# Kernel optimization log

Hardware: AMD Instinct MI355X
Metric: run time of the kernel (lower is better)

Reference implementation:

```python
import jax, jax.numpy as jnp
import numpy as np

N_FFT = 2048
HOP = 441
WIN_SIZE = 7
PAD = WIN_SIZE // 2
NP_WIN = WIN_SIZE * WIN_SIZE
COV_NORM = NP_WIN / (NP_WIN - 1.0)  # sample covariance, skimage default
DATA_RANGE = 2.0  # skimage float dtype_range (-1,1)
C1 = (0.01 * DATA_RANGE) ** 2
C2 = (0.03 * DATA_RANGE) ** 2
EPS = 1e-8

# periodic hann window (librosa fftbins=True)
_HANN = 0.5 - 0.5 * np.cos(2.0 * np.pi * np.arange(N_FFT) / N_FFT)


def wav_to_spectrogram(x):
    # x: [B, C, S] -> magnitude spectrogram [B, C, T, F]
    pad = N_FFT // 2
    xp = jnp.pad(x, ((0, 0), (0, 0), (pad, pad)), mode='reflect')  # torch 'reflect'
    L = xp.shape[-1]
    n_frames = (L - N_FFT) // HOP + 1
    idx = jnp.arange(n_frames)[:, None] * HOP + jnp.arange(N_FFT)[None, :]
    frames = xp[..., idx] * jnp.asarray(_HANN, xp.dtype)  # [B,C,T,N_FFT]
    spec = jnp.fft.rfft(frames, axis=-1)
    mag = jnp.sqrt(jnp.maximum(spec.real ** 2 + spec.imag ** 2, EPS))
    return mag


def _umean_last(x):
    # 1D uniform mean filter (size 7) along last axis, scipy 'reflect' boundary
    xp = jnp.pad(x, [(0, 0)] * (x.ndim - 1) + [(PAD, PAD)], mode='symmetric')
    cs = jnp.cumsum(xp, axis=-1)
    zero = jnp.zeros(cs.shape[:-1] + (1,), cs.dtype)
    cs = jnp.concatenate([zero, cs], axis=-1)
    return (cs[..., WIN_SIZE:] - cs[..., :-WIN_SIZE]) / WIN_SIZE


def umean2d(x):
    # separable 7x7 uniform filter over last two axes
    x = _umean_last(x)
    x = jnp.swapaxes(_umean_last(jnp.swapaxes(x, -1, -2)), -1, -2)
    return x


def ssim_map_mean(X, Y):
    ux, uy = umean2d(X), umean2d(Y)
    uxx, uyy, uxy = umean2d(X * X), umean2d(Y * Y), umean2d(X * Y)
    vx = COV_NORM * (uxx - ux * ux)
    vy = COV_NORM * (uyy - uy * uy)
    vxy = COV_NORM * (uxy - ux * uy)
    S = ((2 * ux * uy + C1) * (2 * vxy + C2)) / ((ux * ux + uy * uy + C1) * (vx + vy + C2))
    # crop pad on each side (skimage) then mean over the spatial map
    return jnp.mean(S[..., PAD:-PAD, PAD:-PAD], axis=(-2, -1))


def setup_inputs() -> dict:
    key = jax.random.key(0)
    k1, k2 = jax.random.split(key)
    B, C, S = 32, 2, 176400
    output = jax.random.normal(k1, (B, C, S), dtype=jnp.float32)
    target = jax.random.normal(k2, (B, C, S), dtype=jnp.float32)
    return {"output": output, "target": target}


def reference(output, target):
    so = wav_to_spectrogram(output)
    st = wav_to_spectrogram(target)
    res = ssim_map_mean(so, st)  # [B, C]
    return res[..., None, None]  # [B, C, 1, 1]
```

## Files before the change

kernel.cpp:

```cpp
#include <hip/hip_runtime.h>
#include <math.h>

#ifndef M_PI
#define M_PI 3.14159265358979323846
#endif

constexpr int S_LEN    = 176400;
constexpr int NFFT     = 2048;
constexpr int NC       = 1024;
constexpr int HOP_     = 441;
constexpr int T_FRAMES = 401;
constexpr int F_BINS   = 1025;
constexpr int F_STRIDE = 1028;
constexpr int N_CH     = 64;
constexpr float EPS_   = 1e-8f;
constexpr float C1_    = 0.0004f;
constexpr float C2_    = 0.0036f;
constexpr float COV_NORM_ = 49.0f / 48.0f;

constexpr int WIN_OFF  = 0;
constexpr int TWG_OFF  = 2048;
constexpr int UTW_OFF  = 3584;
constexpr int SPEC_OFF = 5696;

constexpr int ROWS_PW   = 16;
constexpr int NCHUNKS_R = 25;
constexpr int BANDS     = 5;
constexpr int BAND_ADV  = 248;

__device__ __forceinline__ int phys(int i) { return i ^ ((i >> 2) & 15) ^ ((i >> 6) & 15); }

__device__ __forceinline__ float2 cadd(float2 a, float2 b){ return make_float2(a.x+b.x, a.y+b.y); }
__device__ __forceinline__ float2 csub(float2 a, float2 b){ return make_float2(a.x-b.x, a.y-b.y); }
__device__ __forceinline__ float2 cmul(float2 a, float2 b){ return make_float2(a.x*b.x-a.y*b.y, a.x*b.y+a.y*b.x); }

__global__ __launch_bounds__(256) void init_tables_kernel(float* __restrict__ ws, float* __restrict__ out) {
    const int idx = blockIdx.x * 256 + threadIdx.x;
    if (idx < 64) out[idx] = 0.0f;
    if (idx < NFFT) {
        ws[WIN_OFF + idx] = 0.5f - 0.5f * cosf((float)(2.0 * M_PI / NFFT) * (float)idx);
    }
    if (idx < 768) {
        float ang = -2.0f * (float)M_PI * (float)idx / (float)NC;
        float s, c; sincosf(ang, &s, &c);
        ws[TWG_OFF + 2*idx] = c; ws[TWG_OFF + 2*idx+1] = s;
    }
    if (idx < F_BINS) {
        float ang = -(float)M_PI * (float)idx / (float)NC;
        float s, c; sincosf(ang, &s, &c);
        ws[UTW_OFF + 2*idx] = c; ws[UTW_OFF + 2*idx+1] = s;
    }
}

__device__ __forceinline__ void r4_dif_inplace(
    float2* __restrict__ A, int r0, int r1, int r2, int r3,
    float2 w1, float2 w2, float2 w3, bool tw)
{
    float2 x0c = A[r0];
    float2 x1c = A[r1];
    float2 x2c = A[r2];
    float2 x3c = A[r3];

    float2 a = cadd(x0c, x2c);
    float2 b = csub(x0c, x2c);
    float2 c = cadd(x1c, x3c);
    float2 d = csub(x1c, x3c);

    float2 y0 = cadd(a, c);
    float2 y2 = csub(a, c);
    float2 y1 = make_float2(b.x + d.y, b.y - d.x);
    float2 y3 = make_float2(b.x - d.y, b.y + d.x);

    A[r0] = y0;
    A[r1] = tw ? cmul(y1, w1) : y1;
    A[r2] = tw ? cmul(y2, w2) : y2;
    A[r3] = tw ? cmul(y3, w3) : y3;
}

__global__ __launch_bounds__(256, 8) void stft_mag_kernel(
    const float* __restrict__ x0, const float* __restrict__ x1,
    float* __restrict__ ws, int ch0, int nch, int swizzle)
{
    __shared__ float2 buf[2 * NC];

    const int tid = threadIdx.x;

    int ch, t;
    if (swizzle) {
        int g = blockIdx.x;
        ch = ch0 + (g & 7) * 8 + ((g >> 3) & 7);
        t  = g >> 6;
    } else {
        t  = blockIdx.x;
        ch = ch0 + blockIdx.y;
    }

    const float* __restrict__ xin0 = x0 + (size_t)ch * S_LEN;
    const float* __restrict__ xin1 = x1 + (size_t)ch * S_LEN;
    const float*  __restrict__ win = ws + WIN_OFF;
    const float2* __restrict__ twg = (const float2*)(ws + TWG_OFF);
    const float2* __restrict__ utw = (const float2*)(ws + UTW_OFF);

    const int base = t * HOP_ - NFFT / 2;
    float* fA0 = (float*)buf;
    float* fA1 = (float*)(buf + NC);
    if (base >= 0 && base + NFFT <= S_LEN) {
        #pragma unroll
        for (int k = 0; k < NFFT / 256; ++k) {
            int n = k * 256 + tid;
            int j = base + n;
            float w = win[n];
            int p = 2 * phys(n >> 1) + (n & 1);
            fA0[p] = xin0[j] * w;
            fA1[p] = xin1[j] * w;
        }
    } else {
        #pragma unroll
        for (int k = 0; k < NFFT / 256; ++k) {
            int n = k * 256 + tid;
            int j = base + n;
            j = (j < 0) ? -j : j;
            j = (j >= S_LEN) ? (2 * S_LEN - 2 - j) : j;
            float w = win[n];
            int p = 2 * phys(n >> 1) + (n & 1);
            fA0[p] = xin0[j] * w;
            fA1[p] = xin1[j] * w;
        }
    }
    __syncthreads();

    #pragma unroll
    for (int s = 0; s < 5; ++s) {
        const int M  = 256 >> (2 * s);
        const int q  = tid & (M - 1);
        const int e  = q << (2 * s);
        const int i0 = 4 * (tid - q) + q;

        const int r0 = phys(i0);
        const int r1 = phys(i0 + M);
        const int r2 = phys(i0 + 2 * M);
        const int r3 = phys(i0 + 3 * M);

        float2 w1, w2, w3;
        if (s < 4) {
            w1 = twg[e];
            w2 = twg[2 * e];
            w3 = twg[3 * e];
        } else {
            w1 = w2 = w3 = make_float2(1.0f, 0.0f);
        }

        r4_dif_inplace(buf,      r0, r1, r2, r3, w1, w2, w3, s < 4);
        r4_dif_inplace(buf + NC, r0, r1, r2, r3, w1, w2, w3, s < 4);

        __syncthreads();
    }

    const size_t perT = (size_t)T_FRAMES * F_STRIDE;
    float* __restrict__ sout0 =
        ws + SPEC_OFF + (size_t)(ch - ch0) * perT + (size_t)t * F_STRIDE;
    float* __restrict__ sout1 = sout0 + (size_t)nch * perT;

    const int R8 = ((tid & 3) << 6) | ((tid & 12) << 2) | ((tid >> 2) & 12) | ((tid >> 6) & 3);

    #pragma unroll
    for (int k = 0; k < 5; ++k) {
        int r = k * 256 + tid;
        if (k < 4 || tid == 0) {
            const int ra = (k < 4) ? ((R8 << 2) | k) : 0;
            const int rn = (NC - r) & (NC - 1);
            const int rb = ((rn & 3) << 8) | ((rn & 12) << 4) | (rn & 48)
                         | ((rn >> 4) & 12) | ((rn >> 8) & 3);
            const int ia = phys(ra);
            const int ib = phys(rb);
            float2 wu = utw[r];

            {
                float2 Zr = buf[ia];
                float2 Zn = buf[ib];
                float Ex = 0.5f * (Zr.x + Zn.x);
                float Ey = 0.5f * (Zr.y - Zn.y);
                float Ox = 0.5f * (Zr.y + Zn.y);
                float Oy = 0.5f * (Zn.x - Zr.x);
                float Xx = Ex + wu.x * Ox - wu.y * Oy;
                float Xy = Ey + wu.x * Oy + wu.y * Ox;
                sout0[r] = sqrtf(fmaxf(Xx * Xx + Xy * Xy, EPS_));
            }
            {
                float2 Zr = buf[NC + ia];
                float2 Zn = buf[NC + ib];
                float Ex = 0.5f * (Zr.x + Zn.x);
                float Ey = 0.5f * (Zr.y - Zn.y);
                float Ox = 0.5f * (Zr.y + Zn.y);
                float Oy = 0.5f * (Zn.x - Zr.x);
                float Xx = Ex + wu.x * Ox - wu.y * Oy;
                float Xy = Ey + wu.x * Oy + wu.y * Ox;
                sout1[r] = sqrtf(fmaxf(Xx * Xx + Xy * Xy, EPS_));
            }
        }
    }
}

#define HWIN7(sarr, W) {                                                     \
    float p0 = sarr[0], p01 = p0 + sarr[1], p012 = p01 + sarr[2],            \
          P = p012 + sarr[3];                                                \
    float a1 = __shfl_down(p012, 1, 64);                                     \
    float A1 = __shfl_down(P,    1, 64);                                     \
    float b0 = __shfl_down(p0,   2, 64);                                     \
    float b1 = __shfl_down(p01,  2, 64);                                     \
    W[0] = P + a1;                                                           \
    W[1] = P - p0 + A1;                                                      \
    W[2] = W[1] - sarr[1] + b0;                                              \
    W[3] = W[2] - sarr[2] + (b1 - b0);                                       \
}

__global__ __launch_bounds__(256) void ssim_kernel(
    const float* __restrict__ ws, float* __restrict__ out,
    int ch0, int nch)
{
    const int tid  = threadIdx.x;
    const int wid  = blockIdx.x * 4 + (tid >> 6);
    const int lane = tid & 63;
    const int total = nch * BANDS * NCHUNKS_R;
    if (wid >= total) return;

    const int cg    = wid / (BANDS * NCHUNKS_R);
    const int rem   = wid - cg * (BANDS * NCHUNKS_R);
    const int band  = rem / NCHUNKS_R;
    const int chunk = rem - band * NCHUNKS_R;

    const int t0 = 3 + chunk * ROWS_PW;
    const int t1 = min(t0 + ROWS_PW, T_FRAMES - 3);

    const int cb = band * BAND_ADV;
    int c4 = cb + 4 * lane;
    if (c4 > 1024) c4 = 1024;

    const size_t perT = (size_t)T_FRAMES * F_STRIDE;
    const float* __restrict__ X = ws + SPEC_OFF + (size_t)cg * perT + c4;
    const float* __restrict__ Y = ws + SPEC_OFF + ((size_t)nch + cg) * perT + c4;

    const int  fo      = cb + 3 + 4 * lane;
    const bool lane_ok = (lane <= 61);
    const float inv49  = 1.0f / 49.0f;

    float sx[4] = {0,0,0,0}, sy[4] = {0,0,0,0}, sxx[4] = {0,0,0,0},
          syy[4] = {0,0,0,0}, sxy[4] = {0,0,0,0};

    for (int rr = t0 - 3; rr < t0 + 3; ++rr) {
        float4 xv = *(const float4*)(X + (size_t)rr * F_STRIDE);
        float4 yv = *(const float4*)(Y + (size_t)rr * F_STRIDE);
        float xa[4] = {xv.x, xv.y, xv.z, xv.w}, ya[4] = {yv.x, yv.y, yv.z, yv.w};
        #pragma unroll
        for (int c = 0; c < 4; ++c) {
            sx[c] += xa[c]; sy[c] += ya[c];
            sxx[c] += xa[c]*xa[c]; syy[c] += ya[c]*ya[c]; sxy[c] += xa[c]*ya[c];
        }
    }

    double acc = 0.0;

    #pragma unroll 1
    for (int t = t0; t < t1; ++t) {
        {
            float4 xv = *(const float4*)(X + (size_t)(t + 3) * F_STRIDE);
            float4 yv = *(const float4*)(Y + (size_t)(t + 3) * F_STRIDE);
            float xa[4] = {xv.x, xv.y, xv.z, xv.w}, ya[4] = {yv.x, yv.y, yv.z, yv.w};
            #pragma unroll
            for (int c = 0; c < 4; ++c) {
                sx[c] += xa[c]; sy[c] += ya[c];
                sxx[c] += xa[c]*xa[c]; syy[c] += ya[c]*ya[c]; sxy[c] += xa[c]*ya[c];
            }
        }

        float wx[4], wy[4], wxx[4], wyy[4], wxy[4];
        HWIN7(sx,  wx);
        HWIN7(sy,  wy);
        HWIN7(sxx, wxx);
        HWIN7(syy, wyy);
        HWIN7(sxy, wxy);

        #pragma unroll
        for (int c = 0; c < 4; ++c) {
            if (lane_ok && (fo + c <= 1021)) {
                float ux  = wx[c]  * inv49, uy  = wy[c]  * inv49;
                float uxx = wxx[c] * inv49, uyy = wyy[c] * inv49, uxy = wxy[c] * inv49;
                float vx  = COV_NORM_ * (uxx - ux * ux);
                float vy  = COV_NORM_ * (uyy - uy * uy);
                float vxy = COV_NORM_ * (uxy - ux * uy);
                float Sv = ((2.f * ux * uy + C1_) * (2.f * vxy + C2_)) /
                           ((ux * ux + uy * uy + C1_) * (vx + vy + C2_));
                acc += (double)Sv;
            }
        }

        {
            float4 xv = *(const float4*)(X + (size_t)(t - 3) * F_STRIDE);
            float4 yv = *(const float4*)(Y + (size_t)(t - 3) * F_STRIDE);
            float xa[4] = {xv.x, xv.y, xv.z, xv.w}, ya[4] = {yv.x, yv.y, yv.z, yv.w};
            #pragma unroll
            for (int c = 0; c < 4; ++c) {
                sx[c] -= xa[c]; sy[c] -= ya[c];
                sxx[c] -= xa[c]*xa[c]; syy[c] -= ya[c]*ya[c]; sxy[c] -= xa[c]*ya[c];
            }
        }
    }

    #pragma unroll
    for (int off = 32; off > 0; off >>= 1) acc += __shfl_down(acc, off, 64);
    if (lane == 0) {
        atomicAdd(&out[ch0 + cg], (float)(acc / (395.0 * 1019.0)));
    }
}

extern "C" void kernel_launch(void* const* d_in, const int* in_sizes, int n_in,
                              void* d_out, int out_size, void* d_ws, size_t ws_size,
                              hipStream_t stream) {
    const float* x0 = (const float*)d_in[0];
    const float* x1 = (const float*)d_in[1];
    float* out = (float*)d_out;
    float* ws  = (float*)d_ws;

    const size_t table_bytes  = (size_t)SPEC_OFF * sizeof(float);
    const size_t per_ch_bytes = (size_t)2 * T_FRAMES * F_STRIDE * sizeof(float);
    int G = (int)((ws_size - table_bytes) / per_ch_bytes);
    if (G > N_CH) G = N_CH;
    if (G < 1)    G = 1;

    init_tables_kernel<<<dim3(16), dim3(256), 0, stream>>>(ws, out);

    for (int ch0 = 0; ch0 < N_CH; ch0 += G) {
        const int nch = (N_CH - ch0 < G) ? (N_CH - ch0) : G;

        if (nch == 64) {
            stft_mag_kernel<<<dim3(T_FRAMES * 64), dim3(256), 0, stream>>>(x0, x1, ws, ch0, nch, 1);
        } else {
            stft_mag_kernel<<<dim3(T_FRAMES, nch), dim3(256), 0, stream>>>(x0, x1, ws, ch0, nch, 0);
        }

        const int nwaves = nch * BANDS * NCHUNKS_R;
        ssim_kernel<<<dim3((nwaves + 3) / 4), dim3(256), 0, stream>>>(ws, out, ch0, nch);
    }
}
```

Before: 370.8 us.

## Keep sliding-window rows in a register ring and prefetch next row in SSIM kernel

```diff
diff --git a/kernel.cpp b/kernel.cpp
--- a/kernel.cpp
+++ b/kernel.cpp
@@ -23,8 +23,8 @@
 constexpr int UTW_OFF  = 3584;
 constexpr int SPEC_OFF = 5696;
 
-constexpr int ROWS_PW   = 16;
-constexpr int NCHUNKS_R = 25;
+constexpr int ROWS_PW   = 24;
+constexpr int NCHUNKS_R = 17;
 constexpr int BANDS     = 5;
 constexpr int BAND_ADV  = 248;
 
@@ -246,8 +246,11 @@
 
     float sx[4] = {0,0,0,0}, sy[4] = {0,0,0,0}, sxx[4] = {0,0,0,0},
           syy[4] = {0,0,0,0}, sxy[4] = {0,0,0,0};
-
-    for (int rr = t0 - 3; rr < t0 + 3; ++rr) {
+    float rgx[6][4], rgy[6][4];
+
+    #pragma unroll
+    for (int w = 0; w < 6; ++w) {
+        const int rr = t0 - 3 + w;
         float4 xv = *(const float4*)(X + (size_t)rr * F_STRIDE);
         float4 yv = *(const float4*)(Y + (size_t)rr * F_STRIDE);
         float xa[4] = {xv.x, xv.y, xv.z, xv.w}, ya[4] = {yv.x, yv.y, yv.z, yv.w};
@@ -255,54 +258,64 @@
         for (int c = 0; c < 4; ++c) {
             sx[c] += xa[c]; sy[c] += ya[c];
             sxx[c] += xa[c]*xa[c]; syy[c] += ya[c]*ya[c]; sxy[c] += xa[c]*ya[c];
-        }
-    }
+            rgx[w][c] = xa[c]; rgy[w][c] = ya[c];
+        }
+    }
+
+    float4 cxa = *(const float4*)(X + (size_t)(t0 + 3) * F_STRIDE);
+    float4 cya = *(const float4*)(Y + (size_t)(t0 + 3) * F_STRIDE);
 
     double acc = 0.0;
 
     #pragma unroll 1
-    for (int t = t0; t < t1; ++t) {
-        {
-            float4 xv = *(const float4*)(X + (size_t)(t + 3) * F_STRIDE);
-            float4 yv = *(const float4*)(Y + (size_t)(t + 3) * F_STRIDE);
-            float xa[4] = {xv.x, xv.y, xv.z, xv.w}, ya[4] = {yv.x, yv.y, yv.z, yv.w};
+    for (int tb = t0; tb < t1; tb += 6) {
+        #pragma unroll
+        for (int j = 0; j < 6; ++j) {
+            const int t = tb + j;
+            const int tn = min(t + 4, T_FRAMES - 1);
+            float4 nxa = *(const float4*)(X + (size_t)tn * F_STRIDE);
+            float4 nya = *(const float4*)(Y + (size_t)tn * F_STRIDE);
+
+            float xa[4] = {cxa.x, cxa.y, cxa.z, cxa.w};
+            float ya[4] = {cya.x, cya.y, cya.z, cya.w};
+
             #pragma unroll
             for (int c = 0; c < 4; ++c) {
                 sx[c] += xa[c]; sy[c] += ya[c];
                 sxx[c] += xa[c]*xa[c]; syy[c] += ya[c]*ya[c]; sxy[c] += xa[c]*ya[c];
             }
-        }
-
-        float wx[4], wy[4], wxx[4], wyy[4], wxy[4];
-        HWIN7(sx,  wx);
-        HWIN7(sy,  wy);
-        HWIN7(sxx, wxx);
-        HWIN7(syy, wyy);
-        HWIN7(sxy, wxy);
-
-        #pragma unroll
-        for (int c = 0; c < 4; ++c) {
-            if (lane_ok && (fo + c <= 1021)) {
-                float ux  = wx[c]  * inv49, uy  = wy[c]  * inv49;
-                float uxx = wxx[c] * inv49, uyy = wyy[c] * inv49, uxy = wxy[c] * inv49;
-                float vx  = COV_NORM_ * (uxx - ux * ux);
-                float vy  = COV_NORM_ * (uyy - uy * uy);
-                float vxy = COV_NORM_ * (uxy - ux * uy);
-                float Sv = ((2.f * ux * uy + C1_) * (2.f * vxy + C2_)) /
-                           ((ux * ux + uy * uy + C1_) * (vx + vy + C2_));
-                acc += (double)Sv;
-            }
-        }
-
-        {
-            float4 xv = *(const float4*)(X + (size_t)(t - 3) * F_STRIDE);
-            float4 yv = *(const float4*)(Y + (size_t)(t - 3) * F_STRIDE);
-            float xa[4] = {xv.x, xv.y, xv.z, xv.w}, ya[4] = {yv.x, yv.y, yv.z, yv.w};
+
+            float wx[4], wy[4], wxx[4], wyy[4], wxy[4];
+            HWIN7(sx,  wx);
+            HWIN7(sy,  wy);
+            HWIN7(sxx, wxx);
+            HWIN7(syy, wyy);
+            HWIN7(sxy, wxy);
+
+            const bool live = (t < t1);
             #pragma unroll
             for (int c = 0; c < 4; ++c) {
-                sx[c] -= xa[c]; sy[c] -= ya[c];
-                sxx[c] -= xa[c]*xa[c]; syy[c] -= ya[c]*ya[c]; sxy[c] -= xa[c]*ya[c];
-            }
+                if (live && lane_ok && (fo + c <= 1021)) {
+                    float ux  = wx[c]  * inv49, uy  = wy[c]  * inv49;
+                    float uxx = wxx[c] * inv49, uyy = wyy[c] * inv49, uxy = wxy[c] * inv49;
+                    float vx  = COV_NORM_ * (uxx - ux * ux);
+                    float vy  = COV_NORM_ * (uyy - uy * uy);
+                    float vxy = COV_NORM_ * (uxy - ux * uy);
+                    float Sv = ((2.f * ux * uy + C1_) * (2.f * vxy + C2_)) /
+                               ((ux * ux + uy * uy + C1_) * (vx + vy + C2_));
+                    acc += (double)Sv;
+                }
+            }
+
+            #pragma unroll
+            for (int c = 0; c < 4; ++c) {
+                float bx_ = rgx[j][c], by_ = rgy[j][c];
+                sx[c]  -= bx_;      sy[c]  -= by_;
+                sxx[c] -= bx_*bx_;  syy[c] -= by_*by_;  sxy[c] -= bx_*by_;
+                rgx[j][c] = xa[c];  rgy[j][c] = ya[c];
+            }
+
+            cxa = nxa; cya = nya;
         }
     }
 
```

After: 344.1 us. 7.2% less time.
